# Optimization experiments

Measured on AMD Instinct MI355X. Metric: run time of the kernel, lower is better.

## Reference

```python
import jax, jax.numpy as jnp
import numpy as np

N_NODES = 50000
N_EDGES = 800000


def gcn_conv(x, edge_index, W, b, num_nodes):
    # PyG GCNConv: out = D^-1/2 (A + I) D^-1/2 (X W) + b, with added self-loops.
    xw = x @ W  # [N, F_out]
    src, dst = edge_index[0], edge_index[1]
    loop = jnp.arange(num_nodes, dtype=src.dtype)
    src = jnp.concatenate([src, loop])
    dst = jnp.concatenate([dst, loop])
    # degree (unweighted, after self-loops) on destination nodes
    deg = jax.ops.segment_sum(jnp.ones_like(dst, dtype=xw.dtype), dst,
                              num_segments=num_nodes)
    dinv = jnp.where(deg > 0, jax.lax.rsqrt(deg), 0.0)
    norm = dinv[src] * dinv[dst]  # [E+N]
    msgs = xw[src] * norm[:, None]  # gather + scale
    out = jax.ops.segment_sum(msgs, dst, num_segments=num_nodes)  # scatter-add
    return out + b


def setup_inputs() -> dict:
    key = jax.random.key(0)
    k1, k2, k3, k4 = jax.random.split(key, 4)
    x = jax.random.normal(k1, (N_NODES, 1100), dtype=jnp.float32)
    edge_index = jax.random.randint(k2, (2, N_EDGES), 0, N_NODES, dtype=jnp.int64)
    W1 = jax.random.normal(k3, (512, 256), dtype=jnp.float32) * (1.0 / np.sqrt(512))
    b1 = jnp.zeros((256,), dtype=jnp.float32)
    W2 = jax.random.normal(k4, (256, 128), dtype=jnp.float32) * (1.0 / np.sqrt(256))
    b2 = jnp.zeros((128,), dtype=jnp.float32)
    return {"x": x, "edge_index": edge_index, "W1": W1, "b1": b1,
            "W2": W2, "b2": b2}


def reference(x, edge_index, W1, b1, W2, b2):
    protein_feature = x[:, 588:]  # [N, 512]
    h = gcn_conv(protein_feature, edge_index, W1, b1, N_NODES)
    h = jax.nn.relu(h)
    return gcn_conv(h, edge_index, W2, b2, N_NODES)
```

## Files before the change

### kernel.cpp

```cpp
#include <hip/hip_runtime.h>
#include <hip/hip_bf16.h>
#include <stdint.h>

#define N_NODES 50000
#define N_EDGES 800000

typedef __attribute__((ext_vector_type(8))) __bf16 bf16x8;
typedef __attribute__((ext_vector_type(4))) float floatx4;

__device__ __forceinline__ unsigned short f2bf(float f) {
    union { float f; unsigned u; } v; v.f = f;
    unsigned r = v.u + 0x7fffu + ((v.u >> 16) & 1u);
    return (unsigned short)(r >> 16);
}
__device__ __forceinline__ float bf2f(unsigned short h) {
    union { unsigned u; float f; } v; v.u = ((unsigned)h) << 16;
    return v.f;
}

__global__ __launch_bounds__(256) void count_deg_kernel(
    const int* __restrict__ dst, unsigned* __restrict__ cnt, int nE)
{
    int i = blockIdx.x * blockDim.x + threadIdx.x;
    if (i < nE) {
        unsigned d = (unsigned)dst[i];
        if (d < N_NODES) atomicAdd(&cnt[d], 1u);
    }
}

__global__ __launch_bounds__(256) void dinv_kernel(
    const unsigned* __restrict__ cnt, float* __restrict__ dinv, int n)
{
    int i = blockIdx.x * blockDim.x + threadIdx.x;
    if (i < n) dinv[i] = rsqrtf((float)(cnt[i] + 1u));
}

__global__ __launch_bounds__(256) void block_reduce_kernel(
    const unsigned* __restrict__ cnt, unsigned* __restrict__ blockSums, int n)
{
    __shared__ unsigned s[256];
    int b = blockIdx.x;
    int base = b * 1024;
    unsigned v = 0;
    for (int i = threadIdx.x; i < 1024; i += 256) {
        int idx = base + i;
        v += (idx < n) ? cnt[idx] : 0u;
    }
    s[threadIdx.x] = v; __syncthreads();
    for (int st = 128; st > 0; st >>= 1) {
        if (threadIdx.x < st) s[threadIdx.x] += s[threadIdx.x + st];
        __syncthreads();
    }
    if (threadIdx.x == 0) blockSums[b] = s[0];
}

__global__ __launch_bounds__(64) void scan_sums_kernel(
    unsigned* __restrict__ blockSums, unsigned* __restrict__ off, int nb, int n)
{
    __shared__ unsigned s[64];
    int t = threadIdx.x;
    unsigned v = (t < nb) ? blockSums[t] : 0u;
    s[t] = v; __syncthreads();
    for (int st = 1; st < 64; st <<= 1) {
        unsigned add = (t >= st) ? s[t - st] : 0u;
        __syncthreads();
        s[t] += add;
        __syncthreads();
    }
    if (t < nb) blockSums[t] = s[t] - v;
    if (t == 0) off[n] = s[63];
}

__global__ __launch_bounds__(1024) void block_scan_kernel(
    const unsigned* __restrict__ cnt, const unsigned* __restrict__ blockSums,
    unsigned* __restrict__ off, int n)
{
    __shared__ unsigned s[1024];
    int b = blockIdx.x, t = threadIdx.x;
    int i = b * 1024 + t;
    unsigned v = (i < n) ? cnt[i] : 0u;
    s[t] = v; __syncthreads();
    for (int st = 1; st < 1024; st <<= 1) {
        unsigned add = (t >= st) ? s[t - st] : 0u;
        __syncthreads();
        s[t] += add;
        __syncthreads();
    }
    if (i < n) off[i] = blockSums[b] + s[t] - v;
}

__global__ __launch_bounds__(256) void fill_csr_kernel(
    const int* __restrict__ src, const int* __restrict__ dst,
    const unsigned* __restrict__ off, unsigned* __restrict__ cursor,
    int* __restrict__ csr_src, int nE)
{
    int i = blockIdx.x * blockDim.x + threadIdx.x;
    if (i < nE) {
        unsigned d = (unsigned)dst[i];
        unsigned s = (unsigned)src[i];
        if (d < N_NODES && s < N_NODES) {
            unsigned slot = off[d] + atomicAdd(&cursor[d], 1u);
            csr_src[slot] = (int)s;
        }
    }
}

__global__ __launch_bounds__(256) void split_w_kernel(
    const float* __restrict__ W, unsigned short* __restrict__ Th,
    unsigned short* __restrict__ Tl, int K, int N)
{
    int i = blockIdx.x * blockDim.x + threadIdx.x;
    if (i < K * N) {
        int k = i / N;
        int n = i - k * N;
        float w = W[i];
        unsigned short hi = f2bf(w);
        unsigned short lo = f2bf(w - bf2f(hi));
        Th[(size_t)n * K + k] = hi;
        Tl[(size_t)n * K + k] = lo;
    }
}

#define GBM 128
#define GBN 128
#define GBK 32

__device__ __forceinline__ int chunk_off(int row, int q) {
    return row * 32 + ((q ^ ((row >> 1) & 3)) << 3);
}

template<bool AFP32>
__global__ __launch_bounds__(256) void gemm_mfma_kernel(
    const float* __restrict__ Afp, int lda,
    const unsigned short* __restrict__ Ah, const unsigned short* __restrict__ Al, int apitch,
    const unsigned short* __restrict__ BTh, const unsigned short* __restrict__ BTl,
    const float* __restrict__ dinv, float* __restrict__ Y,
    int M, int K, int N)
{
    __shared__ unsigned short sAh[GBM * GBK];
    __shared__ unsigned short sAl[GBM * GBK];
    __shared__ unsigned short sBh[GBN * GBK];
    __shared__ unsigned short sBl[GBN * GBK];

    const int t    = threadIdx.x;
    const int bm   = blockIdx.x * GBM;
    const int bn   = blockIdx.y * GBN;
    const int w    = t >> 6;
    const int lane = t & 63;
    const int wx   = w & 1;
    const int wy   = w >> 1;
    const int ml   = lane & 15;
    const int quad = lane >> 4;

    const int sr = t >> 1;
    const int q0 = (t & 1) * 2;

    floatx4 zero4 = {0.f, 0.f, 0.f, 0.f};
    floatx4 acc[4][4];
    #pragma unroll
    for (int i = 0; i < 4; ++i)
        #pragma unroll
        for (int j = 0; j < 4; ++j) acc[i][j] = zero4;

    for (int k0 = 0; k0 < K; k0 += GBK) {
        if (AFP32) {
            int gr = bm + sr;
            #pragma unroll
            for (int c = 0; c < 2; ++c) {
                int q = q0 + c;
                float4 v0, v1;
                if (gr < M) {
                    const float* ap = Afp + (size_t)gr * lda + k0 + q * 8;
                    v0 = *(const float4*)(ap);
                    v1 = *(const float4*)(ap + 4);
                } else {
                    v0 = make_float4(0.f,0.f,0.f,0.f);
                    v1 = make_float4(0.f,0.f,0.f,0.f);
                }
                union { unsigned short us[8]; uint4 v; } ph, pl;
                float f[8] = {v0.x, v0.y, v0.z, v0.w, v1.x, v1.y, v1.z, v1.w};
                #pragma unroll
                for (int e = 0; e < 8; ++e) {
                    unsigned short hi = f2bf(f[e]);
                    ph.us[e] = hi;
                    pl.us[e] = f2bf(f[e] - bf2f(hi));
                }
                int off = chunk_off(sr, q);
                *(uint4*)&sAh[off] = ph.v;
                *(uint4*)&sAl[off] = pl.v;
            }
        } else {
            int gr = bm + sr;
            #pragma unroll
            for (int c = 0; c < 2; ++c) {
                int q = q0 + c;
                uint4 vh, vl;
                if (gr < M) {
                    vh = *(const uint4*)(Ah + (size_t)gr * apitch + k0 + q * 8);
                    vl = *(const uint4*)(Al + (size_t)gr * apitch + k0 + q * 8);
                } else {
                    vh = make_uint4(0,0,0,0);
                    vl = make_uint4(0,0,0,0);
                }
                int off = chunk_off(sr, q);
                *(uint4*)&sAh[off] = vh;
                *(uint4*)&sAl[off] = vl;
            }
        }
        {
            int nr = sr;
            const unsigned short* bh = BTh + (size_t)(bn + nr) * K + k0;
            const unsigned short* bl = BTl + (size_t)(bn + nr) * K + k0;
            #pragma unroll
            for (int c = 0; c < 2; ++c) {
                int q = q0 + c;
                uint4 vh = *(const uint4*)(bh + q * 8);
                uint4 vl = *(const uint4*)(bl + q * 8);
                int off = chunk_off(nr, q);
                *(uint4*)&sBh[off] = vh;
                *(uint4*)&sBl[off] = vl;
            }
        }
        __syncthreads();

        bf16x8 fAh[4], fAl[4], fBh[4], fBl[4];
        #pragma unroll
        for (int i = 0; i < 4; ++i) {
            int row = wy * 64 + i * 16 + ml;
            int off = chunk_off(row, quad);
            fAh[i] = *(const bf16x8*)&sAh[off];
            fAl[i] = *(const bf16x8*)&sAl[off];
        }
        #pragma unroll
        for (int j = 0; j < 4; ++j) {
            int nrow = wx * 64 + j * 16 + ml;
            int off = chunk_off(nrow, quad);
            fBh[j] = *(const bf16x8*)&sBh[off];
            fBl[j] = *(const bf16x8*)&sBl[off];
        }

        #pragma unroll
        for (int i = 0; i < 4; ++i)
            #pragma unroll
            for (int j = 0; j < 4; ++j) {
                floatx4 c = acc[i][j];
                c = __builtin_amdgcn_mfma_f32_16x16x32_bf16(fAh[i], fBh[j], c, 0, 0, 0);
                c = __builtin_amdgcn_mfma_f32_16x16x32_bf16(fAl[i], fBh[j], c, 0, 0, 0);
                c = __builtin_amdgcn_mfma_f32_16x16x32_bf16(fAh[i], fBl[j], c, 0, 0, 0);
                acc[i][j] = c;
            }
        __syncthreads();
    }

    #pragma unroll
    for (int i = 0; i < 4; ++i) {
        int rb = bm + wy * 64 + i * 16 + quad * 4;
        float sc[4];
        #pragma unroll
        for (int r = 0; r < 4; ++r) sc[r] = (rb + r < M) ? dinv[rb + r] : 0.f;
        #pragma unroll
        for (int j = 0; j < 4; ++j) {
            int col = bn + wx * 64 + j * 16 + ml;
            #pragma unroll
            for (int r = 0; r < 4; ++r) {
                int grow = rb + r;
                if (grow < M) Y[(size_t)grow * N + col] = acc[i][j][r] * sc[r];
            }
        }
    }
}

__global__ __launch_bounds__(256) void aggregate256_kernel(
    const float* __restrict__ Y, const int* __restrict__ csr_src,
    const unsigned* __restrict__ off, const float* __restrict__ dinv,
    const float* __restrict__ bias,
    unsigned short* __restrict__ Hh, unsigned short* __restrict__ Hl)
{
    const int v  = blockIdx.x * 4 + (threadIdx.x >> 6);
    const int f0 = (threadIdx.x & 63) * 4;

    float4 a0 = *(const float4*)(Y + (size_t)v * 256 + f0);
    float4 a1 = make_float4(0.f,0.f,0.f,0.f);
    float4 a2 = make_float4(0.f,0.f,0.f,0.f);
    float4 a3 = make_float4(0.f,0.f,0.f,0.f);

    const unsigned e0 = off[v], e1 = off[v + 1];
    unsigned j = e0;
    for (; j + 4 <= e1; j += 4) {
        int u0 = csr_src[j + 0];
        int u1 = csr_src[j + 1];
        int u2 = csr_src[j + 2];
        int u3 = csr_src[j + 3];
        float4 m0 = *(const float4*)(Y + (size_t)u0 * 256 + f0);
        float4 m1 = *(const float4*)(Y + (size_t)u1 * 256 + f0);
        float4 m2 = *(const float4*)(Y + (size_t)u2 * 256 + f0);
        float4 m3 = *(const float4*)(Y + (size_t)u3 * 256 + f0);
        a0.x += m0.x; a0.y += m0.y; a0.z += m0.z; a0.w += m0.w;
        a1.x += m1.x; a1.y += m1.y; a1.z += m1.z; a1.w += m1.w;
        a2.x += m2.x; a2.y += m2.y; a2.z += m2.z; a2.w += m2.w;
        a3.x += m3.x; a3.y += m3.y; a3.z += m3.z; a3.w += m3.w;
    }
    for (; j < e1; ++j) {
        float4 m = *(const float4*)(Y + (size_t)csr_src[j] * 256 + f0);
        a0.x += m.x; a0.y += m.y; a0.z += m.z; a0.w += m.w;
    }
    float sx = (a0.x + a1.x) + (a2.x + a3.x);
    float sy = (a0.y + a1.y) + (a2.y + a3.y);
    float sz = (a0.z + a1.z) + (a2.z + a3.z);
    float sw = (a0.w + a1.w) + (a2.w + a3.w);

    float dv = dinv[v];
    float4 b = *(const float4*)(bias + f0);
    float r[4];
    r[0] = fmaxf(sx * dv + b.x, 0.f);
    r[1] = fmaxf(sy * dv + b.y, 0.f);
    r[2] = fmaxf(sz * dv + b.z, 0.f);
    r[3] = fmaxf(sw * dv + b.w, 0.f);

    union { unsigned short us[4]; ushort4 v4; } ph, pl;
    #pragma unroll
    for (int e = 0; e < 4; ++e) {
        unsigned short hi = f2bf(r[e]);
        ph.us[e] = hi;
        pl.us[e] = f2bf(r[e] - bf2f(hi));
    }
    *(ushort4*)(Hh + (size_t)v * 256 + f0) = ph.v4;
    *(ushort4*)(Hl + (size_t)v * 256 + f0) = pl.v4;
}

__global__ __launch_bounds__(256) void aggregate128_kernel(
    const float* __restrict__ Y, const int* __restrict__ csr_src,
    const unsigned* __restrict__ off, const float* __restrict__ dinv,
    const float* __restrict__ bias, float* __restrict__ out)
{
    const int v  = blockIdx.x * 4 + (threadIdx.x >> 6);
    const int f0 = (threadIdx.x & 63) * 2;

    float2 a0 = *(const float2*)(Y + (size_t)v * 128 + f0);
    float2 a1 = make_float2(0.f,0.f);
    float2 a2 = make_float2(0.f,0.f);
    float2 a3 = make_float2(0.f,0.f);

    const unsigned e0 = off[v], e1 = off[v + 1];
    unsigned j = e0;
    for (; j + 4 <= e1; j += 4) {
        int u0 = csr_src[j + 0];
        int u1 = csr_src[j + 1];
        int u2 = csr_src[j + 2];
        int u3 = csr_src[j + 3];
        float2 m0 = *(const float2*)(Y + (size_t)u0 * 128 + f0);
        float2 m1 = *(const float2*)(Y + (size_t)u1 * 128 + f0);
        float2 m2 = *(const float2*)(Y + (size_t)u2 * 128 + f0);
        float2 m3 = *(const float2*)(Y + (size_t)u3 * 128 + f0);
        a0.x += m0.x; a0.y += m0.y;
        a1.x += m1.x; a1.y += m1.y;
        a2.x += m2.x; a2.y += m2.y;
        a3.x += m3.x; a3.y += m3.y;
    }
    for (; j < e1; ++j) {
        float2 m = *(const float2*)(Y + (size_t)csr_src[j] * 128 + f0);
        a0.x += m.x; a0.y += m.y;
    }
    float sx = (a0.x + a1.x) + (a2.x + a3.x);
    float sy = (a0.y + a1.y) + (a2.y + a3.y);

    float dv = dinv[v];
    float2 b = *(const float2*)(bias + f0);
    float2 r = make_float2(sx * dv + b.x, sy * dv + b.y);
    *(float2*)(out + (size_t)v * 128 + f0) = r;
}

extern "C" void kernel_launch(void* const* d_in, const int* in_sizes, int n_in,
                              void* d_out, int out_size, void* d_ws, size_t ws_size,
                              hipStream_t stream)
{
    const float* x  = (const float*)d_in[0];
    const int*   ei = (const int*)d_in[1];
    const float* W1 = (const float*)d_in[2];
    const float* b1 = (const float*)d_in[3];
    const float* W2 = (const float*)d_in[4];
    const float* b2 = (const float*)d_in[5];
    float*       out = (float*)d_out;

    const int* e_src = ei;
    const int* e_dst = ei + N_EDGES;

    char* ws = (char*)d_ws;
    size_t o = 0;
    auto carve = [&](size_t bytes) -> char* {
        char* p = ws + o;
        o = (o + bytes + 511) & ~(size_t)511;
        return p;
    };
    unsigned*       cnt    = (unsigned*)carve((size_t)N_NODES * 4);
    unsigned*       cursor = (unsigned*)carve((size_t)N_NODES * 4);
    unsigned*       off    = (unsigned*)carve((size_t)(N_NODES + 1) * 4);
    unsigned*       bsums  = (unsigned*)carve(64 * 4);
    float*          dinv   = (float*)carve((size_t)N_NODES * 4);
    int*            csr    = (int*)carve((size_t)N_EDGES * 4);
    unsigned short* WT1h   = (unsigned short*)carve((size_t)512 * 256 * 2);
    unsigned short* WT1l   = (unsigned short*)carve((size_t)512 * 256 * 2);
    unsigned short* WT2h   = (unsigned short*)carve((size_t)256 * 128 * 2);
    unsigned short* WT2l   = (unsigned short*)carve((size_t)256 * 128 * 2);
    float*          y      = (float*)carve((size_t)N_NODES * 256 * 4);
    unsigned short* Hh     = (unsigned short*)carve((size_t)N_NODES * 256 * 2);
    unsigned short* Hl     = (unsigned short*)carve((size_t)N_NODES * 256 * 2);
    (void)ws_size;

    hipMemsetAsync(cnt,    0, (size_t)N_NODES * 4, stream);
    hipMemsetAsync(cursor, 0, (size_t)N_NODES * 4, stream);

    const int nScanBlocks = (N_NODES + 1023) / 1024;

    count_deg_kernel<<<(N_EDGES + 255) / 256, 256, 0, stream>>>(e_dst, cnt, N_EDGES);
    dinv_kernel<<<(N_NODES + 255) / 256, 256, 0, stream>>>(cnt, dinv, N_NODES);
    block_reduce_kernel<<<nScanBlocks, 256, 0, stream>>>(cnt, bsums, N_NODES);
    scan_sums_kernel<<<1, 64, 0, stream>>>(bsums, off, nScanBlocks, N_NODES);
    block_scan_kernel<<<nScanBlocks, 1024, 0, stream>>>(cnt, bsums, off, N_NODES);
    fill_csr_kernel<<<(N_EDGES + 255) / 256, 256, 0, stream>>>(e_src, e_dst, off, cursor, csr, N_EDGES);

    split_w_kernel<<<(512 * 256 + 255) / 256, 256, 0, stream>>>(W1, WT1h, WT1l, 512, 256);
    split_w_kernel<<<(256 * 128 + 255) / 256, 256, 0, stream>>>(W2, WT2h, WT2l, 256, 128);

    {
        dim3 grid((N_NODES + GBM - 1) / GBM, 256 / GBN);
        gemm_mfma_kernel<true><<<grid, 256, 0, stream>>>(
            x + 588, 1100, nullptr, nullptr, 0, WT1h, WT1l, dinv, y,
            N_NODES, 512, 256);
    }
    aggregate256_kernel<<<N_NODES / 4, 256, 0, stream>>>(y, csr, off, dinv, b1, Hh, Hl);

    {
        dim3 grid((N_NODES + GBM - 1) / GBM, 128 / GBN);
        gemm_mfma_kernel<false><<<grid, 256, 0, stream>>>(
            nullptr, 0, Hh, Hl, 256, WT2h, WT2l, dinv, y,
            N_NODES, 256, 128);
    }
    aggregate128_kernel<<<N_NODES / 4, 256, 0, stream>>>(y, csr, off, dinv, b2, out);
}
```

Measured before the change: 659.5 us.

## Pre-split x into bf16 hi/lo, fuse dinv into scan, unroll aggregation by 8

Adds a split_x_kernel that converts the 512-column slice of x into bf16 hi/lo arrays once, so the layer-1 GEMM no longer reads fp32 and splits it twice (once per N-tile block column). The dinv computation moves into block_scan_kernel, the two memsets are merged into one covering the adjacent cnt and cursor buffers, and both aggregation kernels gather 8 neighbours per iteration instead of 4. The trade-off is an extra pass that writes and rereads about 100MB of bf16 data, which may cost more than the removed redundant conversion.

```diff
diff --git a/kernel.cpp b/kernel.cpp
--- a/kernel.cpp
+++ b/kernel.cpp
@@ -26,13 +26,6 @@
         unsigned d = (unsigned)dst[i];
         if (d < N_NODES) atomicAdd(&cnt[d], 1u);
     }
-}
-
-__global__ __launch_bounds__(256) void dinv_kernel(
-    const unsigned* __restrict__ cnt, float* __restrict__ dinv, int n)
-{
-    int i = blockIdx.x * blockDim.x + threadIdx.x;
-    if (i < n) dinv[i] = rsqrtf((float)(cnt[i] + 1u));
 }
 
 __global__ __launch_bounds__(256) void block_reduce_kernel(
@@ -73,7 +66,7 @@
 
 __global__ __launch_bounds__(1024) void block_scan_kernel(
     const unsigned* __restrict__ cnt, const unsigned* __restrict__ blockSums,
-    unsigned* __restrict__ off, int n)
+    unsigned* __restrict__ off, float* __restrict__ dinv, int n)
 {
     __shared__ unsigned s[1024];
     int b = blockIdx.x, t = threadIdx.x;
@@ -86,7 +79,10 @@
         s[t] += add;
         __syncthreads();
     }
-    if (i < n) off[i] = blockSums[b] + s[t] - v;
+    if (i < n) {
+        off[i]  = blockSums[b] + s[t] - v;
+        dinv[i] = rsqrtf((float)(v + 1u));
+    }
 }
 
 __global__ __launch_bounds__(256) void fill_csr_kernel(
@@ -121,6 +117,28 @@
     }
 }
 
+__global__ __launch_bounds__(256) void split_x_kernel(
+    const float* __restrict__ x, unsigned short* __restrict__ Xh,
+    unsigned short* __restrict__ Xl)
+{
+    int i = blockIdx.x * 256 + threadIdx.x;
+    int row  = i >> 7;
+    int col4 = (i & 127) << 2;
+    if (row < N_NODES) {
+        float4 v = *(const float4*)(x + (size_t)row * 1100 + 588 + col4);
+        union { unsigned short us[4]; ushort4 v4; } ph, pl;
+        float f[4] = {v.x, v.y, v.z, v.w};
+        #pragma unroll
+        for (int e = 0; e < 4; ++e) {
+            unsigned short hi = f2bf(f[e]);
+            ph.us[e] = hi;
+            pl.us[e] = f2bf(f[e] - bf2f(hi));
+        }
+        *(ushort4*)(Xh + (size_t)row * 512 + col4) = ph.v4;
+        *(ushort4*)(Xl + (size_t)row * 512 + col4) = pl.v4;
+    }
+}
+
 #define GBM 128
 #define GBN 128
 #define GBK 32
@@ -129,9 +147,7 @@
     return row * 32 + ((q ^ ((row >> 1) & 3)) << 3);
 }
 
-template<bool AFP32>
 __global__ __launch_bounds__(256) void gemm_mfma_kernel(
-    const float* __restrict__ Afp, int lda,
     const unsigned short* __restrict__ Ah, const unsigned short* __restrict__ Al, int apitch,
     const unsigned short* __restrict__ BTh, const unsigned short* __restrict__ BTl,
     const float* __restrict__ dinv, float* __restrict__ Y,
@@ -163,33 +179,7 @@
         for (int j = 0; j < 4; ++j) acc[i][j] = zero4;
 
     for (int k0 = 0; k0 < K; k0 += GBK) {
-        if (AFP32) {
-            int gr = bm + sr;
-            #pragma unroll
-            for (int c = 0; c < 2; ++c) {
-                int q = q0 + c;
-                float4 v0, v1;
-                if (gr < M) {
-                    const float* ap = Afp + (size_t)gr * lda + k0 + q * 8;
-                    v0 = *(const float4*)(ap);
-                    v1 = *(const float4*)(ap + 4);
-                } else {
-                    v0 = make_float4(0.f,0.f,0.f,0.f);
-                    v1 = make_float4(0.f,0.f,0.f,0.f);
-                }
-                union { unsigned short us[8]; uint4 v; } ph, pl;
-                float f[8] = {v0.x, v0.y, v0.z, v0.w, v1.x, v1.y, v1.z, v1.w};
-                #pragma unroll
-                for (int e = 0; e < 8; ++e) {
-                    unsigned short hi = f2bf(f[e]);
-                    ph.us[e] = hi;
-                    pl.us[e] = f2bf(f[e] - bf2f(hi));
-                }
-                int off = chunk_off(sr, q);
-                *(uint4*)&sAh[off] = ph.v;
-                *(uint4*)&sAl[off] = pl.v;
-            }
-        } else {
+        {
             int gr = bm + sr;
             #pragma unroll
             for (int c = 0; c < 2; ++c) {
@@ -208,15 +198,14 @@
             }
         }
         {
-            int nr = sr;
-            const unsigned short* bh = BTh + (size_t)(bn + nr) * K + k0;
-            const unsigned short* bl = BTl + (size_t)(bn + nr) * K + k0;
+            const unsigned short* bh = BTh + (size_t)(bn + sr) * K + k0;
+            const unsigned short* bl = BTl + (size_t)(bn + sr) * K + k0;
             #pragma unroll
             for (int c = 0; c < 2; ++c) {
                 int q = q0 + c;
                 uint4 vh = *(const uint4*)(bh + q * 8);
                 uint4 vl = *(const uint4*)(bl + q * 8);
-                int off = chunk_off(nr, q);
+                int off = chunk_off(sr, q);
                 *(uint4*)&sBh[off] = vh;
                 *(uint4*)&sBl[off] = vl;
             }
@@ -286,19 +275,20 @@
 
     const unsigned e0 = off[v], e1 = off[v + 1];
     unsigned j = e0;
-    for (; j + 4 <= e1; j += 4) {
-        int u0 = csr_src[j + 0];
-        int u1 = csr_src[j + 1];
-        int u2 = csr_src[j + 2];
-        int u3 = csr_src[j + 3];
-        float4 m0 = *(const float4*)(Y + (size_t)u0 * 256 + f0);
-        float4 m1 = *(const float4*)(Y + (size_t)u1 * 256 + f0);
-        float4 m2 = *(const float4*)(Y + (size_t)u2 * 256 + f0);
-        float4 m3 = *(const float4*)(Y + (size_t)u3 * 256 + f0);
-        a0.x += m0.x; a0.y += m0.y; a0.z += m0.z; a0.w += m0.w;
-        a1.x += m1.x; a1.y += m1.y; a1.z += m1.z; a1.w += m1.w;
-        a2.x += m2.x; a2.y += m2.y; a2.z += m2.z; a2.w += m2.w;
-        a3.x += m3.x; a3.y += m3.y; a3.z += m3.z; a3.w += m3.w;
+    for (; j + 8 <= e1; j += 8) {
+        int u[8];
+        #pragma unroll
+        for (int q = 0; q < 8; ++q) u[q] = csr_src[j + q];
+        float4 m[8];
+        #pragma unroll
+        for (int q = 0; q < 8; ++q) m[q] = *(const float4*)(Y + (size_t)u[q] * 256 + f0);
+        #pragma unroll
+        for (int q = 0; q < 8; q += 4) {
+            a0.x += m[q+0].x; a0.y += m[q+0].y; a0.z += m[q+0].z; a0.w += m[q+0].w;
+            a1.x += m[q+1].x; a1.y += m[q+1].y; a1.z += m[q+1].z; a1.w += m[q+1].w;
+            a2.x += m[q+2].x; a2.y += m[q+2].y; a2.z += m[q+2].z; a2.w += m[q+2].w;
+            a3.x += m[q+3].x; a3.y += m[q+3].y; a3.z += m[q+3].z; a3.w += m[q+3].w;
+        }
     }
     for (; j < e1; ++j) {
         float4 m = *(const float4*)(Y + (size_t)csr_src[j] * 256 + f0);
@@ -343,19 +333,20 @@
 
     const unsigned e0 = off[v], e1 = off[v + 1];
     unsigned j = e0;
-    for (; j + 4 <= e1; j += 4) {
-        int u0 = csr_src[j + 0];
-        int u1 = csr_src[j + 1];
-        int u2 = csr_src[j + 2];
-        int u3 = csr_src[j + 3];
-        float2 m0 = *(const float2*)(Y + (size_t)u0 * 128 + f0);
-        float2 m1 = *(const float2*)(Y + (size_t)u1 * 128 + f0);
-        float2 m2 = *(const float2*)(Y + (size_t)u2 * 128 + f0);
-        float2 m3 = *(const float2*)(Y + (size_t)u3 * 128 + f0);
-        a0.x += m0.x; a0.y += m0.y;
-        a1.x += m1.x; a1.y += m1.y;
-        a2.x += m2.x; a2.y += m2.y;
-        a3.x += m3.x; a3.y += m3.y;
+    for (; j + 8 <= e1; j += 8) {
+        int u[8];
+        #pragma unroll
+        for (int q = 0; q < 8; ++q) u[q] = csr_src[j + q];
+        float2 m[8];
+        #pragma unroll
+        for (int q = 0; q < 8; ++q) m[q] = *(const float2*)(Y + (size_t)u[q] * 128 + f0);
+        #pragma unroll
+        for (int q = 0; q < 8; q += 4) {
+            a0.x += m[q+0].x; a0.y += m[q+0].y;
+            a1.x += m[q+1].x; a1.y += m[q+1].y;
+            a2.x += m[q+2].x; a2.y += m[q+2].y;
+            a3.x += m[q+3].x; a3.y += m[q+3].y;
+        }
     }
     for (; j < e1; ++j) {
         float2 m = *(const float2*)(Y + (size_t)csr_src[j] * 128 + f0);
@@ -402,39 +393,39 @@
     unsigned short* WT1l   = (unsigned short*)carve((size_t)512 * 256 * 2);
     unsigned short* WT2h   = (unsigned short*)carve((size_t)256 * 128 * 2);
     unsigned short* WT2l   = (unsigned short*)carve((size_t)256 * 128 * 2);
+    unsigned short* Xh     = (unsigned short*)carve((size_t)N_NODES * 512 * 2);
+    unsigned short* Xl     = (unsigned short*)carve((size_t)N_NODES * 512 * 2);
     float*          y      = (float*)carve((size_t)N_NODES * 256 * 4);
     unsigned short* Hh     = (unsigned short*)carve((size_t)N_NODES * 256 * 2);
     unsigned short* Hl     = (unsigned short*)carve((size_t)N_NODES * 256 * 2);
     (void)ws_size;
 
-    hipMemsetAsync(cnt,    0, (size_t)N_NODES * 4, stream);
-    hipMemsetAsync(cursor, 0, (size_t)N_NODES * 4, stream);
+    size_t cntAligned = ((size_t)N_NODES * 4 + 511) & ~(size_t)511;
+    hipMemsetAsync(cnt, 0, cntAligned + (size_t)N_NODES * 4, stream);
 
     const int nScanBlocks = (N_NODES + 1023) / 1024;
 
     count_deg_kernel<<<(N_EDGES + 255) / 256, 256, 0, stream>>>(e_dst, cnt, N_EDGES);
-    dinv_kernel<<<(N_NODES + 255) / 256, 256, 0, stream>>>(cnt, dinv, N_NODES);
     block_reduce_kernel<<<nScanBlocks, 256, 0, stream>>>(cnt, bsums, N_NODES);
     scan_sums_kernel<<<1, 64, 0, stream>>>(bsums, off, nScanBlocks, N_NODES);
-    block_scan_kernel<<<nScanBlocks, 1024, 0, stream>>>(cnt, bsums, off, N_NODES);
+    block_scan_kernel<<<nScanBlocks, 1024, 0, stream>>>(cnt, bsums, off, dinv, N_NODES);
     fill_csr_kernel<<<(N_EDGES + 255) / 256, 256, 0, stream>>>(e_src, e_dst, off, cursor, csr, N_EDGES);
 
     split_w_kernel<<<(512 * 256 + 255) / 256, 256, 0, stream>>>(W1, WT1h, WT1l, 512, 256);
     split_w_kernel<<<(256 * 128 + 255) / 256, 256, 0, stream>>>(W2, WT2h, WT2l, 256, 128);
+    split_x_kernel<<<(N_NODES * 128 + 255) / 256, 256, 0, stream>>>(x, Xh, Xl);
 
     {
         dim3 grid((N_NODES + GBM - 1) / GBM, 256 / GBN);
-        gemm_mfma_kernel<true><<<grid, 256, 0, stream>>>(
-            x + 588, 1100, nullptr, nullptr, 0, WT1h, WT1l, dinv, y,
-            N_NODES, 512, 256);
+        gemm_mfma_kernel<<<grid, 256, 0, stream>>>(
+            Xh, Xl, 512, WT1h, WT1l, dinv, y, N_NODES, 512, 256);
     }
     aggregate256_kernel<<<N_NODES / 4, 256, 0, stream>>>(y, csr, off, dinv, b1, Hh, Hl);
 
     {
         dim3 grid((N_NODES + GBM - 1) / GBM, 128 / GBN);
-        gemm_mfma_kernel<false><<<grid, 256, 0, stream>>>(
-            nullptr, 0, Hh, Hl, 256, WT2h, WT2l, dinv, y,
-            N_NODES, 256, 128);
+        gemm_mfma_kernel<<<grid, 256, 0, stream>>>(
+            Hh, Hl, 256, WT2h, WT2l, dinv, y, N_NODES, 256, 128);
     }
     aggregate128_kernel<<<N_NODES / 4, 256, 0, stream>>>(y, csr, off, dinv, b2, out);
 }
```

After: 665.7 us. Within noise of the previous version (+0.9%).
